# Kernel optimization log

Measured on AMD Instinct MI355X. Metric: run time of the kernel, lower is better.

## Reference

```python
import jax, jax.numpy as jnp
import numpy as np

B, N, D = 4, 2048, 1024
HEADS, DIM_HEAD = 16, 64
INNER = HEADS * DIM_HEAD  # 1024
SCALE = DIM_HEAD ** -0.5


def setup_inputs() -> dict:
    key = jax.random.key(0)
    ks = jax.random.split(key, 8)
    w = 0.02
    return {
        "x":  jax.random.normal(ks[0], (B, N, D), dtype=jnp.float32),
        "Wq": jax.random.normal(ks[1], (D, INNER), dtype=jnp.float32) * w,
        "bq": jax.random.normal(ks[2], (INNER,), dtype=jnp.float32) * w,
        "Wv": jax.random.normal(ks[3], (D, INNER), dtype=jnp.float32) * w,
        "bv": jax.random.normal(ks[4], (INNER,), dtype=jnp.float32) * w,
        "Wo": jax.random.normal(ks[5], (INNER, D), dtype=jnp.float32) * w,
        "bo": jax.random.normal(ks[6], (D,), dtype=jnp.float32) * w,
    }


def reference(x, Wq, bq, Wv, bv, Wo, bo):
    b, n, _ = x.shape
    q = x @ Wq + bq                      # [b, n, inner]
    v = x @ Wv + bv                      # [b, n, inner]
    # split heads -> [b, h, n, d]
    q = q.reshape(b, n, HEADS, DIM_HEAD).transpose(0, 2, 1, 3).astype(jnp.float32)
    v = v.reshape(b, n, HEADS, DIM_HEAD).transpose(0, 2, 1, 3)
    # k = q (self L2 attention)
    AB = jnp.einsum('bhid,bhjd->bhij', q, q)          # [b, h, n, n]
    AA = jnp.sum(q * q, axis=-1, keepdims=True)       # [b, h, n, 1]
    BB = jnp.swapaxes(AA, -1, -2)                     # [b, h, 1, n]
    sim = -(AA - 2.0 * AB + BB) * SCALE               # negative scaled L2 distance
    attn = jax.nn.softmax(sim, axis=-1)
    out = jnp.einsum('bhij,bhjd->bhid', attn, v)      # [b, h, n, d]
    out = out.transpose(0, 2, 1, 3).reshape(b, n, INNER)
    return out @ Wo + bo
```

## Files before the change

kernel.cpp:

```cpp
#include <hip/hip_runtime.h>
#include <hip/hip_bf16.h>

#define SEQ 2048
#define SCALE 0.125f
#define LOG2E 1.4426950408889634f
#define ALPHA 0.6005612049f

typedef __bf16 bf16;
typedef __bf16 bf16x4 __attribute__((ext_vector_type(4)));
typedef __bf16 bf16x8 __attribute__((ext_vector_type(8)));
typedef _Float16 f16;
typedef _Float16 f16x2 __attribute__((ext_vector_type(2)));
typedef _Float16 f16x4 __attribute__((ext_vector_type(4)));
typedef _Float16 f16x8 __attribute__((ext_vector_type(8)));
typedef float f32x4 __attribute__((ext_vector_type(4)));
typedef unsigned int u32;
typedef unsigned int u32x2 __attribute__((ext_vector_type(2)));
typedef unsigned int u32x4 __attribute__((ext_vector_type(4)));

__device__ __forceinline__ f16x2 pk_f16(float a, float b) {
    return __builtin_bit_cast(f16x2, __builtin_amdgcn_cvt_pkrtz(a, b));
}

__device__ __forceinline__ u32 pk_u32(float a, float b) {
    return __builtin_bit_cast(u32, __builtin_amdgcn_cvt_pkrtz(a, b));
}

__device__ __forceinline__ f32x4 mfma_f16_32(f16x8 a, f16x8 b, f32x4 c) {
    return __builtin_amdgcn_mfma_f32_16x16x32_f16(a, b, c, 0, 0, 0);
}

__device__ __forceinline__ void gl_lds16(const void* g, void* l) {
    __builtin_amdgcn_global_load_lds((const __attribute__((address_space(1))) u32*)g,
                                     (__attribute__((address_space(3))) u32*)l, 16, 0, 0);
}


__global__ __launch_bounds__(256) void k_cast_x(const float4* __restrict__ x,
                                                bf16x4* __restrict__ xb) {
    int t = blockIdx.x * 256 + threadIdx.x;
    float4 f = x[t];
    bf16x4 o;
    o[0] = (bf16)f.x; o[1] = (bf16)f.y; o[2] = (bf16)f.z; o[3] = (bf16)f.w;
    xb[t] = o;
}

__global__ __launch_bounds__(256) void k_transpose_cast(const float* __restrict__ src,
                                                        bf16* __restrict__ dst) {
    __shared__ float tile[32][33];
    int bx = blockIdx.x * 32;
    int by = blockIdx.y * 32;
    int tx = threadIdx.x;
    int ty = threadIdx.y;
#pragma unroll
    for (int j = 0; j < 32; j += 8)
        tile[ty + j][tx] = src[(size_t)(by + ty + j) * 1024 + bx + tx];
    __syncthreads();
#pragma unroll
    for (int j = 0; j < 32; j += 8)
        dst[(size_t)(bx + ty + j) * 1024 + by + tx] = (bf16)tile[tx][ty + j];
}


__global__ __launch_bounds__(256) void k_gemm_qv(const bf16* __restrict__ Xb,
                                                 const bf16* __restrict__ Wqvt,
                                                 const float* __restrict__ bq,
                                                 const float* __restrict__ bv,
                                                 bf16* __restrict__ Q,
                                                 f16* __restrict__ Vt,
                                                 float* __restrict__ QN) {
    constexpr int K = 1024;
    __shared__ bf16 As[128 * 32];
    __shared__ bf16 Bs[128 * 32];
    int t = threadIdx.x, w = t >> 6, l = t & 63;
    int blockN = blockIdx.x * 128, blockM = blockIdx.y * 128;
    int wm = w & 1, wn = w >> 1;
    int lr = l & 15, quad = l >> 4, q8 = quad * 8;
    int skcol = (l & 3) * 8;
    bool isQ = blockN < 1024;

    f32x4 acc[4][4] = {};
    const bf16* Ab = Xb + (size_t)blockM * K;
    const bf16* Bb = Wqvt + (size_t)blockN * K;

    for (int k0 = 0; k0 < K; k0 += 32) {
#pragma unroll
        for (int c2 = 0; c2 < 2; ++c2) {
            int c = 2 * w + c2;
            int row = c * 16 + (l >> 2);
            gl_lds16(Ab + (size_t)row * K + k0 + skcol, As + c * 512);
            gl_lds16(Bb + (size_t)row * K + k0 + skcol, Bs + c * 512);
        }
        __syncthreads();
        const bf16* Aw = As + wm * 64 * 32;
        const bf16* Bw = Bs + wn * 64 * 32;
        bf16x8 af[4], bfr[4];
#pragma unroll
        for (int mi = 0; mi < 4; ++mi) af[mi] = *(const bf16x8*)(Aw + (mi * 16 + lr) * 32 + q8);
#pragma unroll
        for (int ni = 0; ni < 4; ++ni) bfr[ni] = *(const bf16x8*)(Bw + (ni * 16 + lr) * 32 + q8);
        if (isQ) {
#pragma unroll
            for (int mi = 0; mi < 4; ++mi)
#pragma unroll
                for (int ni = 0; ni < 4; ++ni)
                    acc[mi][ni] = __builtin_amdgcn_mfma_f32_16x16x32_bf16(af[mi], bfr[ni], acc[mi][ni], 0, 0, 0);
        } else {
#pragma unroll
            for (int mi = 0; mi < 4; ++mi)
#pragma unroll
                for (int ni = 0; ni < 4; ++ni)
                    acc[mi][ni] = __builtin_amdgcn_mfma_f32_16x16x32_bf16(bfr[ni], af[mi], acc[mi][ni], 0, 0, 0);
        }
        __syncthreads();
    }

    int colbase = blockN + wn * 64;
    if (isQ) {
        int h = colbase >> 6;
        float bias[4];
#pragma unroll
        for (int ni = 0; ni < 4; ++ni) bias[ni] = bq[colbase + ni * 16 + lr];
#pragma unroll
        for (int mi = 0; mi < 4; ++mi) {
#pragma unroll
            for (int r = 0; r < 4; ++r) {
                int m = blockM + wm * 64 + mi * 16 + quad * 4 + r;
                int b = m >> 11, s = m & 2047;
                int bh = (b << 4) + h;
                float qsq = 0.f;
#pragma unroll
                for (int ni = 0; ni < 4; ++ni) {
                    float v = (acc[mi][ni][r] + bias[ni]) * ALPHA;
                    bf16 vb = (bf16)v;
                    Q[((size_t)bh * SEQ + s) * 64 + ni * 16 + lr] = vb;
                    float vr = (float)vb;
                    qsq += vr * vr;
                }
                qsq += __shfl_xor(qsq, 1);
                qsq += __shfl_xor(qsq, 2);
                qsq += __shfl_xor(qsq, 4);
                qsq += __shfl_xor(qsq, 8);
                if (lr == 0) QN[(size_t)bh * SEQ + s] = -0.5f * qsq;
            }
        }
    } else {
        int h = (colbase - 1024) >> 6;
        int b = blockM >> 11;
        int bh = (b << 4) + h;
        int s_base = (blockM & 2047) + wm * 64;
        const float* bvh = bv + (colbase - 1024);
#pragma unroll
        for (int ni = 0; ni < 4; ++ni) {
#pragma unroll
            for (int r = 0; r < 4; ++r) {
                int dh = ni * 16 + quad * 4 + r;
                float bias = bvh[dh];
#pragma unroll
                for (int mi = 0; mi < 4; ++mi) {
                    int s = s_base + mi * 16 + lr;
                    Vt[((size_t)bh * 64 + dh) * SEQ + s] = (f16)(acc[mi][ni][r] + bias);
                }
            }
        }
    }
}


__global__ __launch_bounds__(256, 4) void k_attn(const bf16* __restrict__ Q,
                                                 const f16* __restrict__ Vt,
                                                 const float* __restrict__ QN,
                                                 bf16* __restrict__ AO) {
    __shared__ bf16 Ks[64 * 64];
    __shared__ f16 Vs[64 * 64];
    __shared__ float BBl[2048];

    int t = threadIdx.x, w = t >> 6, l = t & 63;
    int bh = blockIdx.y;
    int i0 = blockIdx.x * 128;
    const bf16* Qh = Q + (size_t)bh * SEQ * 64;
    const f16* Vh = Vt + (size_t)bh * 64 * SEQ;
    int lr = l & 15, quad = l >> 4, q8 = quad * 8, lr7 = lr & 7;

    {
        const float4* QN4 = (const float4*)(QN + (size_t)bh * SEQ);
        float4* BB4 = (float4*)BBl;
        BB4[t] = QN4[t];
        BB4[t + 256] = QN4[t + 256];
    }

    bf16x8 af[2][2];
#pragma unroll
    for (int mi = 0; mi < 2; ++mi)
#pragma unroll
        for (int kc = 0; kc < 2; ++kc)
            af[mi][kc] = *(const bf16x8*)(Qh + (size_t)(i0 + w * 32 + mi * 16 + lr) * 64 + kc * 32 + q8);

    f32x4 oacc[2][4] = {};
    f32x4 dacc[2] = {};
    const f16x8 ones8 = {(f16)1.f, (f16)1.f, (f16)1.f, (f16)1.f,
                         (f16)1.f, (f16)1.f, (f16)1.f, (f16)1.f};

    int kb[2];
#pragma unroll
    for (int kc = 0; kc < 2; ++kc) kb[kc] = lr * 64 + (((kc * 4 + quad) ^ lr7) * 8);
    int voff[4];
#pragma unroll
    for (int di = 0; di < 4; ++di) voff[di] = (di * 16 + lr) * 64;
    int npo[2];
#pragma unroll
    for (int np = 0; np < 2; ++np) npo[np] = ((np * 4 + quad) ^ lr7) * 8;

    int sr0 = t >> 3, sc = t & 7;
    int sr1 = sr0 + 32;
    int sl0 = sr0 * 64 + ((sc ^ (sr0 & 7)) * 8);
    int sl1 = sr1 * 64 + ((sc ^ (sr1 & 7)) * 8);

    u32x4 rk0 = *(const u32x4*)(Qh + (size_t)sr0 * 64 + sc * 8);
    u32x4 rk1 = *(const u32x4*)(Qh + (size_t)sr1 * 64 + sc * 8);
    u32x4 rv0 = *(const u32x4*)(Vh + (size_t)sr0 * SEQ + sc * 8);
    u32x4 rv1 = *(const u32x4*)(Vh + (size_t)sr1 * SEQ + sc * 8);

    for (int j0 = 0; j0 < SEQ; j0 += 64) {
        __syncthreads();
        *(u32x4*)(Ks + sl0) = rk0;
        *(u32x4*)(Ks + sl1) = rk1;
        *(u32x4*)(Vs + sl0) = rv0;
        *(u32x4*)(Vs + sl1) = rv1;
        int jn = j0 + 64;
        if (jn < SEQ) {
            rk0 = *(const u32x4*)(Qh + (size_t)(jn + sr0) * 64 + sc * 8);
            rk1 = *(const u32x4*)(Qh + (size_t)(jn + sr1) * 64 + sc * 8);
            rv0 = *(const u32x4*)(Vh + (size_t)sr0 * SEQ + jn + sc * 8);
            rv1 = *(const u32x4*)(Vh + (size_t)sr1 * SEQ + jn + sc * 8);
        }
        __syncthreads();

#pragma unroll
        for (int np = 0; np < 2; ++np) {
            u32 hA[2][2], hB[2][2];
#pragma unroll
            for (int ni1 = 0; ni1 < 2; ++ni1) {
                int ni = np * 2 + ni1;
                bf16x8 bk0 = *(const bf16x8*)(Ks + ni * 1024 + kb[0]);
                bf16x8 bk1 = *(const bf16x8*)(Ks + ni * 1024 + kb[1]);
                f32x4 bbt = *(const f32x4*)(BBl + j0 + ni * 16 + quad * 4);
                f32x4 sT0 = bbt, sT1 = bbt;
                sT0 = __builtin_amdgcn_mfma_f32_16x16x32_bf16(bk0, af[0][0], sT0, 0, 0, 0);
                sT0 = __builtin_amdgcn_mfma_f32_16x16x32_bf16(bk1, af[0][1], sT0, 0, 0, 0);
                sT1 = __builtin_amdgcn_mfma_f32_16x16x32_bf16(bk0, af[1][0], sT1, 0, 0, 0);
                sT1 = __builtin_amdgcn_mfma_f32_16x16x32_bf16(bk1, af[1][1], sT1, 0, 0, 0);

                float p00 = __builtin_amdgcn_exp2f(sT0[0]);
                float p01 = __builtin_amdgcn_exp2f(sT0[1]);
                float p02 = __builtin_amdgcn_exp2f(sT0[2]);
                float p03 = __builtin_amdgcn_exp2f(sT0[3]);
                float p10 = __builtin_amdgcn_exp2f(sT1[0]);
                float p11 = __builtin_amdgcn_exp2f(sT1[1]);
                float p12 = __builtin_amdgcn_exp2f(sT1[2]);
                float p13 = __builtin_amdgcn_exp2f(sT1[3]);

                hA[ni1][0] = pk_u32(p00, p01);
                hA[ni1][1] = pk_u32(p02, p03);
                hB[ni1][0] = pk_u32(p10, p11);
                hB[ni1][1] = pk_u32(p12, p13);
            }
            f16x8 F8[2];
            {
                u32 a0 = hA[0][0], b0 = hA[1][0], a1 = hA[0][1], b1 = hA[1][1];
                asm("v_permlane32_swap_b32 %0, %1" : "+v"(a0), "+v"(b0));
                asm("v_permlane16_swap_b32 %0, %1" : "+v"(a0), "+v"(b0));
                asm("v_permlane32_swap_b32 %0, %1" : "+v"(a1), "+v"(b1));
                asm("v_permlane16_swap_b32 %0, %1" : "+v"(a1), "+v"(b1));
                u32x4 fu = {a0, a1, b0, b1};
                F8[0] = __builtin_bit_cast(f16x8, fu);
            }
            {
                u32 a0 = hB[0][0], b0 = hB[1][0], a1 = hB[0][1], b1 = hB[1][1];
                asm("v_permlane32_swap_b32 %0, %1" : "+v"(a0), "+v"(b0));
                asm("v_permlane16_swap_b32 %0, %1" : "+v"(a0), "+v"(b0));
                asm("v_permlane32_swap_b32 %0, %1" : "+v"(a1), "+v"(b1));
                asm("v_permlane16_swap_b32 %0, %1" : "+v"(a1), "+v"(b1));
                u32x4 fu = {a0, a1, b0, b1};
                F8[1] = __builtin_bit_cast(f16x8, fu);
            }

            dacc[0] = mfma_f16_32(F8[0], ones8, dacc[0]);
            dacc[1] = mfma_f16_32(F8[1], ones8, dacc[1]);

#pragma unroll
            for (int di = 0; di < 4; ++di) {
                f16x8 vf8 = *(const f16x8*)(Vs + voff[di] + npo[np]);
                oacc[0][di] = mfma_f16_32(F8[0], vf8, oacc[0][di]);
                oacc[1][di] = mfma_f16_32(F8[1], vf8, oacc[1][di]);
            }
        }
    }

    int b = bh >> 4, h = bh & 15;
#pragma unroll
    for (int mi = 0; mi < 2; ++mi) {
#pragma unroll
        for (int r = 0; r < 4; ++r) {
            float inv = 1.f / dacc[mi][r];
            int s = i0 + w * 32 + mi * 16 + quad * 4 + r;
#pragma unroll
            for (int di = 0; di < 4; ++di) {
                AO[((size_t)(b * SEQ + s)) * 1024 + h * 64 + di * 16 + lr] = (bf16)(oacc[mi][di][r] * inv);
            }
        }
    }
}


__global__ __launch_bounds__(256) void k_gemm_out(const bf16* __restrict__ AO,
                                                  const bf16* __restrict__ Wot,
                                                  const float* __restrict__ bo,
                                                  float* __restrict__ out) {
    constexpr int K = 1024;
    __shared__ bf16 As[128 * 32];
    __shared__ bf16 Bs[128 * 32];
    int t = threadIdx.x, w = t >> 6, l = t & 63;
    int blockN = blockIdx.x * 128, blockM = blockIdx.y * 128;
    int wm = w & 1, wn = w >> 1;
    int lr = l & 15, quad = l >> 4, q8 = quad * 8;
    int skcol = (l & 3) * 8;

    f32x4 acc[4][4] = {};
    const bf16* Ab = AO + (size_t)blockM * K;
    const bf16* Bb = Wot + (size_t)blockN * K;

    for (int k0 = 0; k0 < K; k0 += 32) {
#pragma unroll
        for (int c2 = 0; c2 < 2; ++c2) {
            int c = 2 * w + c2;
            int row = c * 16 + (l >> 2);
            gl_lds16(Ab + (size_t)row * K + k0 + skcol, As + c * 512);
            gl_lds16(Bb + (size_t)row * K + k0 + skcol, Bs + c * 512);
        }
        __syncthreads();
        const bf16* Aw = As + wm * 64 * 32;
        const bf16* Bw = Bs + wn * 64 * 32;
        bf16x8 af[4], bfr[4];
#pragma unroll
        for (int mi = 0; mi < 4; ++mi) af[mi] = *(const bf16x8*)(Aw + (mi * 16 + lr) * 32 + q8);
#pragma unroll
        for (int ni = 0; ni < 4; ++ni) bfr[ni] = *(const bf16x8*)(Bw + (ni * 16 + lr) * 32 + q8);
#pragma unroll
        for (int mi = 0; mi < 4; ++mi)
#pragma unroll
            for (int ni = 0; ni < 4; ++ni)
                acc[mi][ni] = __builtin_amdgcn_mfma_f32_16x16x32_bf16(af[mi], bfr[ni], acc[mi][ni], 0, 0, 0);
        __syncthreads();
    }

    int colbase = blockN + wn * 64;
    float bias[4];
#pragma unroll
    for (int ni = 0; ni < 4; ++ni) bias[ni] = bo[colbase + ni * 16 + lr];
#pragma unroll
    for (int mi = 0; mi < 4; ++mi) {
#pragma unroll
        for (int r = 0; r < 4; ++r) {
            int m = blockM + wm * 64 + mi * 16 + quad * 4 + r;
#pragma unroll
            for (int ni = 0; ni < 4; ++ni) {
                out[(size_t)m * 1024 + colbase + ni * 16 + lr] = acc[mi][ni][r] + bias[ni];
            }
        }
    }
}


extern "C" void kernel_launch(void* const* d_in, const int* in_sizes, int n_in,
                              void* d_out, int out_size, void* d_ws, size_t ws_size,
                              hipStream_t stream) {
    const float* x  = (const float*)d_in[0];
    const float* Wq = (const float*)d_in[1];
    const float* bq = (const float*)d_in[2];
    const float* Wv = (const float*)d_in[3];
    const float* bv = (const float*)d_in[4];
    const float* Wo = (const float*)d_in[5];
    const float* bo = (const float*)d_in[6];
    float* out = (float*)d_out;

    char* ws = (char*)d_ws;
    bf16* Xb   = (bf16*)ws;
    bf16* Wqvt = (bf16*)(ws + (size_t)(16 << 20));
    bf16* Wot  = (bf16*)(ws + (size_t)(20 << 20));
    bf16* Qb   = (bf16*)(ws + (size_t)(22 << 20));
    f16*  Vtb  = (f16*)(ws + (size_t)(38 << 20));
    float* QN  = (float*)(ws + (size_t)(54 << 20));
    bf16* AO   = Xb;

    k_cast_x<<<8192, 256, 0, stream>>>((const float4*)x, (bf16x4*)Xb);
    dim3 tb(32, 8);
    k_transpose_cast<<<dim3(32, 32), tb, 0, stream>>>(Wq, Wqvt);
    k_transpose_cast<<<dim3(32, 32), tb, 0, stream>>>(Wv, Wqvt + 1024 * 1024);
    k_transpose_cast<<<dim3(32, 32), tb, 0, stream>>>(Wo, Wot);
    k_gemm_qv<<<dim3(16, 64), 256, 0, stream>>>(Xb, Wqvt, bq, bv, Qb, Vtb, QN);
    k_attn<<<dim3(16, 64), 256, 0, stream>>>(Qb, Vtb, QN, AO);
    k_gemm_out<<<dim3(8, 64), 256, 0, stream>>>(AO, Wot, bo, out);
}
```

Measured before the change: 275.1 us.

## Double-buffer attention K/V tiles, remap blocks, batch QK MFMAs, merge weight transposes

The attention kernel now keeps two LDS buffers for K and V and writes the next tile while the current one is computed, so each iteration needs one barrier instead of two. It also issues all QK MFMAs for a tile before the exp/pack stage to give the scheduler more independent work. Blocks are remapped so that groups of heads and query blocks that run together share K/V in cache, and the three weight transpose launches are merged into one. The costs are twice the LDS for K/V, which may reduce occupancy, and more live score registers.

```diff
diff --git a/kernel.cpp b/kernel.cpp
--- a/kernel.cpp
+++ b/kernel.cpp
@@ -18,10 +18,6 @@
 typedef unsigned int u32x2 __attribute__((ext_vector_type(2)));
 typedef unsigned int u32x4 __attribute__((ext_vector_type(4)));
 
-__device__ __forceinline__ f16x2 pk_f16(float a, float b) {
-    return __builtin_bit_cast(f16x2, __builtin_amdgcn_cvt_pkrtz(a, b));
-}
-
 __device__ __forceinline__ u32 pk_u32(float a, float b) {
     return __builtin_bit_cast(u32, __builtin_amdgcn_cvt_pkrtz(a, b));
 }
@@ -45,9 +41,15 @@
     xb[t] = o;
 }
 
-__global__ __launch_bounds__(256) void k_transpose_cast(const float* __restrict__ src,
-                                                        bf16* __restrict__ dst) {
+__global__ __launch_bounds__(256) void k_transpose_cast3(const float* __restrict__ Wq,
+                                                         const float* __restrict__ Wv,
+                                                         const float* __restrict__ Wo,
+                                                         bf16* __restrict__ Wqvt,
+                                                         bf16* __restrict__ Wot) {
     __shared__ float tile[32][33];
+    int z = blockIdx.z;
+    const float* src = (z == 0) ? Wq : (z == 1) ? Wv : Wo;
+    bf16* dst = (z == 0) ? Wqvt : (z == 1) ? (Wqvt + 1024 * 1024) : Wot;
     int bx = blockIdx.x * 32;
     int by = blockIdx.y * 32;
     int tx = threadIdx.x;
@@ -171,13 +173,14 @@
                                                  const f16* __restrict__ Vt,
                                                  const float* __restrict__ QN,
                                                  bf16* __restrict__ AO) {
-    __shared__ bf16 Ks[64 * 64];
-    __shared__ f16 Vs[64 * 64];
+    __shared__ bf16 Ks[2][64 * 64];
+    __shared__ f16 Vs[2][64 * 64];
     __shared__ float BBl[2048];
 
     int t = threadIdx.x, w = t >> 6, l = t & 63;
-    int bh = blockIdx.y;
-    int i0 = blockIdx.x * 128;
+    int p = blockIdx.x + (blockIdx.y << 4);
+    int bh = ((p >> 7) << 3) + (p & 7);
+    int i0 = ((p >> 3) & 15) * 128;
     const bf16* Qh = Q + (size_t)bh * SEQ * 64;
     const f16* Vh = Vt + (size_t)bh * 64 * SEQ;
     int lr = l & 15, quad = l >> 4, q8 = quad * 8, lr7 = lr & 7;
@@ -220,81 +223,91 @@
     u32x4 rk1 = *(const u32x4*)(Qh + (size_t)sr1 * 64 + sc * 8);
     u32x4 rv0 = *(const u32x4*)(Vh + (size_t)sr0 * SEQ + sc * 8);
     u32x4 rv1 = *(const u32x4*)(Vh + (size_t)sr1 * SEQ + sc * 8);
+    *(u32x4*)(&Ks[0][sl0]) = rk0;
+    *(u32x4*)(&Ks[0][sl1]) = rk1;
+    *(u32x4*)(&Vs[0][sl0]) = rv0;
+    *(u32x4*)(&Vs[0][sl1]) = rv1;
+    rk0 = *(const u32x4*)(Qh + (size_t)(64 + sr0) * 64 + sc * 8);
+    rk1 = *(const u32x4*)(Qh + (size_t)(64 + sr1) * 64 + sc * 8);
+    rv0 = *(const u32x4*)(Vh + (size_t)sr0 * SEQ + 64 + sc * 8);
+    rv1 = *(const u32x4*)(Vh + (size_t)sr1 * SEQ + 64 + sc * 8);
+    __syncthreads();
 
     for (int j0 = 0; j0 < SEQ; j0 += 64) {
-        __syncthreads();
-        *(u32x4*)(Ks + sl0) = rk0;
-        *(u32x4*)(Ks + sl1) = rk1;
-        *(u32x4*)(Vs + sl0) = rv0;
-        *(u32x4*)(Vs + sl1) = rv1;
+        int cur = (j0 >> 6) & 1;
         int jn = j0 + 64;
         if (jn < SEQ) {
-            rk0 = *(const u32x4*)(Qh + (size_t)(jn + sr0) * 64 + sc * 8);
-            rk1 = *(const u32x4*)(Qh + (size_t)(jn + sr1) * 64 + sc * 8);
-            rv0 = *(const u32x4*)(Vh + (size_t)sr0 * SEQ + jn + sc * 8);
-            rv1 = *(const u32x4*)(Vh + (size_t)sr1 * SEQ + jn + sc * 8);
-        }
-        __syncthreads();
-
-#pragma unroll
-        for (int np = 0; np < 2; ++np) {
-            u32 hA[2][2], hB[2][2];
+            bf16* Kn = &Ks[cur ^ 1][0];
+            f16* Vn = &Vs[cur ^ 1][0];
+            *(u32x4*)(Kn + sl0) = rk0;
+            *(u32x4*)(Kn + sl1) = rk1;
+            *(u32x4*)(Vn + sl0) = rv0;
+            *(u32x4*)(Vn + sl1) = rv1;
+            int j2 = j0 + 128;
+            if (j2 < SEQ) {
+                rk0 = *(const u32x4*)(Qh + (size_t)(j2 + sr0) * 64 + sc * 8);
+                rk1 = *(const u32x4*)(Qh + (size_t)(j2 + sr1) * 64 + sc * 8);
+                rv0 = *(const u32x4*)(Vh + (size_t)sr0 * SEQ + j2 + sc * 8);
+                rv1 = *(const u32x4*)(Vh + (size_t)sr1 * SEQ + j2 + sc * 8);
+            }
+        }
+        const bf16* Kc = &Ks[cur][0];
+        const f16* Vc = &Vs[cur][0];
+
+        f32x4 sT[2][2][2];
+#pragma unroll
+        for (int np = 0; np < 2; ++np)
 #pragma unroll
             for (int ni1 = 0; ni1 < 2; ++ni1) {
                 int ni = np * 2 + ni1;
-                bf16x8 bk0 = *(const bf16x8*)(Ks + ni * 1024 + kb[0]);
-                bf16x8 bk1 = *(const bf16x8*)(Ks + ni * 1024 + kb[1]);
+                bf16x8 bk0 = *(const bf16x8*)(Kc + ni * 1024 + kb[0]);
+                bf16x8 bk1 = *(const bf16x8*)(Kc + ni * 1024 + kb[1]);
                 f32x4 bbt = *(const f32x4*)(BBl + j0 + ni * 16 + quad * 4);
-                f32x4 sT0 = bbt, sT1 = bbt;
-                sT0 = __builtin_amdgcn_mfma_f32_16x16x32_bf16(bk0, af[0][0], sT0, 0, 0, 0);
-                sT0 = __builtin_amdgcn_mfma_f32_16x16x32_bf16(bk1, af[0][1], sT0, 0, 0, 0);
-                sT1 = __builtin_amdgcn_mfma_f32_16x16x32_bf16(bk0, af[1][0], sT1, 0, 0, 0);
-                sT1 = __builtin_amdgcn_mfma_f32_16x16x32_bf16(bk1, af[1][1], sT1, 0, 0, 0);
-
-                float p00 = __builtin_amdgcn_exp2f(sT0[0]);
-                float p01 = __builtin_amdgcn_exp2f(sT0[1]);
-                float p02 = __builtin_amdgcn_exp2f(sT0[2]);
-                float p03 = __builtin_amdgcn_exp2f(sT0[3]);
-                float p10 = __builtin_amdgcn_exp2f(sT1[0]);
-                float p11 = __builtin_amdgcn_exp2f(sT1[1]);
-                float p12 = __builtin_amdgcn_exp2f(sT1[2]);
-                float p13 = __builtin_amdgcn_exp2f(sT1[3]);
-
-                hA[ni1][0] = pk_u32(p00, p01);
-                hA[ni1][1] = pk_u32(p02, p03);
-                hB[ni1][0] = pk_u32(p10, p11);
-                hB[ni1][1] = pk_u32(p12, p13);
-            }
+                f32x4 s0 = __builtin_amdgcn_mfma_f32_16x16x32_bf16(bk0, af[0][0], bbt, 0, 0, 0);
+                s0 = __builtin_amdgcn_mfma_f32_16x16x32_bf16(bk1, af[0][1], s0, 0, 0, 0);
+                f32x4 s1 = __builtin_amdgcn_mfma_f32_16x16x32_bf16(bk0, af[1][0], bbt, 0, 0, 0);
+                s1 = __builtin_amdgcn_mfma_f32_16x16x32_bf16(bk1, af[1][1], s1, 0, 0, 0);
+                sT[np][ni1][0] = s0;
+                sT[np][ni1][1] = s1;
+            }
+
+#pragma unroll
+        for (int np = 0; np < 2; ++np) {
+            u32 h[2][2][2];
+#pragma unroll
+            for (int ni1 = 0; ni1 < 2; ++ni1)
+#pragma unroll
+                for (int mi = 0; mi < 2; ++mi) {
+                    f32x4 s = sT[np][ni1][mi];
+                    float p0 = __builtin_amdgcn_exp2f(s[0]);
+                    float p1 = __builtin_amdgcn_exp2f(s[1]);
+                    float p2 = __builtin_amdgcn_exp2f(s[2]);
+                    float p3 = __builtin_amdgcn_exp2f(s[3]);
+                    h[mi][ni1][0] = pk_u32(p0, p1);
+                    h[mi][ni1][1] = pk_u32(p2, p3);
+                }
             f16x8 F8[2];
-            {
-                u32 a0 = hA[0][0], b0 = hA[1][0], a1 = hA[0][1], b1 = hA[1][1];
+#pragma unroll
+            for (int mi = 0; mi < 2; ++mi) {
+                u32 a0 = h[mi][0][0], b0 = h[mi][1][0], a1 = h[mi][0][1], b1 = h[mi][1][1];
                 asm("v_permlane32_swap_b32 %0, %1" : "+v"(a0), "+v"(b0));
                 asm("v_permlane16_swap_b32 %0, %1" : "+v"(a0), "+v"(b0));
                 asm("v_permlane32_swap_b32 %0, %1" : "+v"(a1), "+v"(b1));
                 asm("v_permlane16_swap_b32 %0, %1" : "+v"(a1), "+v"(b1));
                 u32x4 fu = {a0, a1, b0, b1};
-                F8[0] = __builtin_bit_cast(f16x8, fu);
-            }
-            {
-                u32 a0 = hB[0][0], b0 = hB[1][0], a1 = hB[0][1], b1 = hB[1][1];
-                asm("v_permlane32_swap_b32 %0, %1" : "+v"(a0), "+v"(b0));
-                asm("v_permlane16_swap_b32 %0, %1" : "+v"(a0), "+v"(b0));
-                asm("v_permlane32_swap_b32 %0, %1" : "+v"(a1), "+v"(b1));
-                asm("v_permlane16_swap_b32 %0, %1" : "+v"(a1), "+v"(b1));
-                u32x4 fu = {a0, a1, b0, b1};
-                F8[1] = __builtin_bit_cast(f16x8, fu);
+                F8[mi] = __builtin_bit_cast(f16x8, fu);
             }
 
             dacc[0] = mfma_f16_32(F8[0], ones8, dacc[0]);
             dacc[1] = mfma_f16_32(F8[1], ones8, dacc[1]);
-
 #pragma unroll
             for (int di = 0; di < 4; ++di) {
-                f16x8 vf8 = *(const f16x8*)(Vs + voff[di] + npo[np]);
+                f16x8 vf8 = *(const f16x8*)(Vc + voff[di] + npo[np]);
                 oacc[0][di] = mfma_f16_32(F8[0], vf8, oacc[0][di]);
                 oacc[1][di] = mfma_f16_32(F8[1], vf8, oacc[1][di]);
             }
         }
+        __syncthreads();
     }
 
     int b = bh >> 4, h = bh & 15;
@@ -395,9 +408,7 @@
 
     k_cast_x<<<8192, 256, 0, stream>>>((const float4*)x, (bf16x4*)Xb);
     dim3 tb(32, 8);
-    k_transpose_cast<<<dim3(32, 32), tb, 0, stream>>>(Wq, Wqvt);
-    k_transpose_cast<<<dim3(32, 32), tb, 0, stream>>>(Wv, Wqvt + 1024 * 1024);
-    k_transpose_cast<<<dim3(32, 32), tb, 0, stream>>>(Wo, Wot);
+    k_transpose_cast3<<<dim3(32, 32, 3), tb, 0, stream>>>(Wq, Wv, Wo, Wqvt, Wot);
     k_gemm_qv<<<dim3(16, 64), 256, 0, stream>>>(Xb, Wqvt, bq, bv, Qb, Vtb, QN);
     k_attn<<<dim3(16, 64), 256, 0, stream>>>(Qb, Vtb, QN, AO);
     k_gemm_out<<<dim3(8, 64), 256, 0, stream>>>(AO, Wot, bo, out);
```

Result: no change. 280.0 us (+1.8%).
